# Performance work log

Measured on AMD Instinct MI355X. Metric: run time of the kernel, lower is better.

The kernel has to match this reference:

```python
import jax, jax.numpy as jnp
import numpy as np

T_STEPS = 40        # 30 gated steps + 10 extra steps (original while<30 then for min(10,..))
GATED_STEPS = 30
BATCH = 4096
X_DIM = 150
H_DIM = 150


def setup_inputs() -> dict:
    key = jax.random.key(0)
    ks = jax.random.split(key, 11)
    s = lambda k, shape: jax.random.normal(k, shape, jnp.float32) * 0.05
    return {
        "x": jax.random.normal(ks[0], (T_STEPS, BATCH, X_DIM), jnp.float32),
        "w_ih": s(ks[1], (4 * H_DIM, X_DIM)),
        "w_hh": s(ks[2], (4 * H_DIM, H_DIM)),
        "b_ih": s(ks[3], (4 * H_DIM,)),
        "b_hh": s(ks[4], (4 * H_DIM,)),
        "w1": s(ks[5], (50, X_DIM + H_DIM)),
        "b1": s(ks[6], (50,)),
        "w2": s(ks[7], (25, 50)),
        "b2": s(ks[8], (25,)),
        "w3": s(ks[9], (2, 25)),
        "b3": s(ks[10], (2,)),
    }


def reference(x, w_ih, w_hh, b_ih, b_hh, w1, b1, w2, b2, w3, b3):
    B = x.shape[1]
    H = w_hh.shape[1]

    def cell(h, c, xt):
        # PyTorch LSTMCell: gate order i, f, g, o
        g = xt @ w_ih.T + b_ih + h @ w_hh.T + b_hh  # [B, 4H]
        i, f, gg, o = jnp.split(g, 4, axis=-1)
        c = jax.nn.sigmoid(f) * c + jax.nn.sigmoid(i) * jnp.tanh(gg)
        h = jax.nn.sigmoid(o) * jnp.tanh(c)
        return h, c

    def stop_gate(h, xt):
        # original detaches the concat input (requires_grad=False on .data)
        t = jax.lax.stop_gradient(jnp.concatenate([h, xt], axis=-1))  # [B, 300]
        t = jax.nn.relu(t @ w1.T + b1)
        t = jax.nn.relu(t @ w2.T + b2)
        return jax.nn.softmax(jax.nn.relu(t @ w3.T + b3), axis=-1)  # [B, 2]

    def step_gated(carry, xt):
        h, c = carry
        h, c = cell(h, c, xt)
        y = stop_gate(h, xt)
        return (h, c), (h, y)

    def step_plain(carry, xt):
        h, c = carry
        h, c = cell(h, c, xt)
        return (h, c), h

    h0 = jnp.zeros((B, H), x.dtype)
    c0 = jnp.zeros((B, H), x.dtype)
    (h, c), (hs1, ys) = jax.lax.scan(step_gated, (h0, c0), x[:GATED_STEPS])
    outh = h  # h_t at the end of the gated phase (original `outh`)
    (h, c), hs2 = jax.lax.scan(step_plain, (h, c), x[GATED_STEPS:])
    outputs = jnp.concatenate([hs1, hs2], axis=0)  # [T, B, H]
    return outh, outputs, ys
```

## Files before the change

### kernel.cpp

```cpp
#include <hip/hip_runtime.h>
#include <math.h>

#define TSTEPS 40
#define GATED  30
#define BATCH  4096
#define XD     150
#define HD     150
#define HP     160
#define PITCHW 328
#define SXP    328
#define WROWS  704
#define ROWS   16
#define NT     512
#define NBLK   (BATCH / ROWS)

#define S1P    68
#define S2P    28
#define W2P    52

#define OFF_OUTPUTS 614400
#define OFF_YS      25190400

typedef float  floatx4 __attribute__((ext_vector_type(4)));
typedef short  shortx8 __attribute__((ext_vector_type(8)));

__device__ __forceinline__ unsigned short bf16_rne(float f) {
    union { float f; unsigned int u; } v; v.f = f;
    unsigned int u = v.u;
    return (unsigned short)((u + 0x7fffu + ((u >> 16) & 1u)) >> 16);
}
__device__ __forceinline__ unsigned int pk2bf(float a, float b) {
    return (unsigned int)bf16_rne(a) | ((unsigned int)bf16_rne(b) << 16);
}
__device__ __forceinline__ float rcp_f(float x) {
    return __builtin_amdgcn_rcpf(x);
}
__device__ __forceinline__ float sigf(float x) {
    return rcp_f(1.0f + __expf(-x));
}
__device__ __forceinline__ float tanh_fast(float x) {
    x = fminf(fmaxf(x, -15.0f), 15.0f);
    float t = __expf(2.0f * x);
    return (t - 1.0f) * rcp_f(t + 1.0f);
}
__device__ __forceinline__ void bar_lds() {
    asm volatile("s_waitcnt lgkmcnt(0)\n\ts_barrier" ::: "memory");
}

__global__ void pack_weights(const float* __restrict__ w_ih, const float* __restrict__ w_hh,
                             const float* __restrict__ b_ih, const float* __restrict__ b_hh,
                             const float* __restrict__ w1,
                             unsigned short* __restrict__ Wc, float* __restrict__ bcp) {
    int idx = blockIdx.x * blockDim.x + threadIdx.x;
    int stride = gridDim.x * blockDim.x;
    for (int i = idx; i < WROWS * PITCHW; i += stride) {
        int j = i / PITCHW, k = i - j * PITCHW;
        float v = 0.0f;
        if (j < 640) {
            int tp = j / HP, u = j - tp * HP;
            if (u < 150) {
                int src = tp * 150 + u;
                if (k < 150)                    v = w_ih[src * 150 + k];
                else if (k >= 160 && k < 310)   v = w_hh[src * 150 + (k - 160)];
            }
        } else {
            int j1 = j - 640;
            if (j1 < 50) {
                if (k < 150)                    v = w1[j1 * 300 + 150 + k];
                else if (k >= 160 && k < 310)   v = w1[j1 * 300 + (k - 160)];
            }
        }
        Wc[i] = bf16_rne(v);
    }
    for (int i = idx; i < 640; i += stride) {
        int tp = i / HP, u = i - tp * HP;
        bcp[i] = (u < 150) ? (b_ih[tp * 150 + u] + b_hh[tp * 150 + u]) : 0.0f;
    }
}

__global__ __launch_bounds__(NT, 2)
void lstm_main(const float* __restrict__ x,
               const unsigned short* __restrict__ Wc,
               const float* __restrict__ bcp,
               float* __restrict__ outh, float* __restrict__ outputs) {
    __shared__ unsigned short sxh[2][ROWS][SXP];
    __shared__ float sge[ROWS][4][33];
    __shared__ unsigned short wlds[8][16][SXP];
    __shared__ float bcs[640];

    const int tid  = threadIdx.x;
    const int lane = tid & 63;
    const int wv   = tid >> 6;
    const int lrow = lane & 15;
    const int lq   = lane >> 4;
    const int row0 = blockIdx.x * ROWS;
    const int ty   = wv >> 1;
    const int ch   = wv & 1;

    for (int i = tid; i < 2 * ROWS * SXP; i += NT) {
        int b = i / (ROWS * SXP);
        int rem = i - b * (ROWS * SXP);
        int r = rem / SXP, k = rem - r * SXP;
        if (k >= 150) sxh[b][r][k] = 0;
    }
    for (int i = tid; i < ROWS * 75; i += NT) {
        int rr = i / 75, kk = i - rr * 75;
        float2 v = *(const float2*)(x + ((size_t)row0 + rr) * XD + 2 * kk);
        *(unsigned int*)&sxh[0][rr][2 * kk] = pk2bf(v.x, v.y);
    }
    for (int i = tid; i < 8 * 16 * 160; i += NT) {
        int w = i / (16 * 160);
        int rem = i - w * (16 * 160);
        int r = rem / 160, k = rem - r * 160;
        int et = 10 * (w >> 1) + 8 + (w & 1);
        *(unsigned int*)&wlds[w][r][2 * k] =
            *(const unsigned int*)&Wc[(size_t)(et * 16 + r) * PITCHW + 2 * k];
    }
    for (int i = tid; i < 640; i += NT) bcs[i] = bcp[i];

    shortx8 bfr[40];
#pragma unroll
    for (int j = 0; j < 4; ++j) {
        const unsigned short* wp =
            Wc + (size_t)((10 * j + wv) * 16 + lrow) * PITCHW + lq * 8;
#pragma unroll
        for (int kb = 0; kb < 10; ++kb)
            bfr[j * 10 + kb] = *(const shortx8*)(wp + kb * 32);
    }

    __syncthreads();

    const int uq = wv * 16 + lrow;
    const float bcq0 = bcs[uq];
    const float bcq1 = bcs[160 + uq];
    const float bcq2 = bcs[320 + uq];
    const float bcq3 = bcs[480 + uq];
    const int ce_c = tid & 31;
    const int ue = 128 + ce_c;
    const int re = tid >> 5;
    const float bce0 = bcs[ue];
    const float bce1 = bcs[160 + ue];
    const float bce2 = bcs[320 + ue];
    const float bce3 = bcs[480 + ue];
    const int pr0 = tid / 75,          pk0 = tid % 75;
    const int pr1 = (tid + 512) / 75,  pk1 = (tid + 512) % 75;
    const int pr2 = (tid + 1024) / 75, pk2 = (tid + 1024) % 75;

    float* outc = outputs + (size_t)(row0 + lq * 4) * HD + uq;

    float cr[4] = {0.f, 0.f, 0.f, 0.f};
    float cex = 0.f;

    unsigned short (*sxc)[SXP] = sxh[0];
    unsigned short (*sxn)[SXP] = sxh[1];

    for (int t = 0; t < TSTEPS; ++t) {
        float2 px0, px1, px2;
        const bool pf = (t + 1 < TSTEPS);
        if (pf) {
            const float* xn = x + ((size_t)(t + 1) * BATCH + row0) * XD;
            px0 = *(const float2*)(xn + pr0 * XD + 2 * pk0);
            px1 = *(const float2*)(xn + pr1 * XD + 2 * pk1);
            if (tid < 176) px2 = *(const float2*)(xn + pr2 * XD + 2 * pk2);
        }

        float ge0, ge1, ge2, ge3;
        if (t > 0) {
            ge0 = sge[re][0][ce_c];
            ge1 = sge[re][1][ce_c];
            ge2 = sge[re][2][ce_c];
            ge3 = sge[re][3][ce_c];
        }

        floatx4 acc[5];
#pragma unroll
        for (int j = 0; j < 5; ++j) acc[j] = (floatx4){0.f, 0.f, 0.f, 0.f};
#pragma unroll
        for (int kb = 0; kb < 9; ++kb) {
            shortx8 a = *(const shortx8*)&sxc[lrow][kb * 32 + lq * 8];
#pragma unroll
            for (int j = 0; j < 4; ++j)
                acc[j] = __builtin_amdgcn_mfma_f32_16x16x32_bf16(
                    a, bfr[j * 10 + kb], acc[j], 0, 0, 0);
            shortx8 b4 = *(const shortx8*)&wlds[wv][lrow][kb * 32 + lq * 8];
            acc[4] = __builtin_amdgcn_mfma_f32_16x16x32_bf16(a, b4, acc[4], 0, 0, 0);
        }

        if (t > 0) {
            float gi = ge0 + bce0;
            float gf = ge1 + bce1;
            float gg = ge2 + bce2;
            float go = ge3 + bce3;
            float cn = sigf(gf) * cex + sigf(gi) * tanh_fast(gg);
            cex = cn;
            float h = sigf(go) * tanh_fast(cn);
            sxc[re][HP + ue] = bf16_rne(h);
            if (ue < 150) {
                outputs[((size_t)(t - 1) * BATCH + row0 + re) * HD + ue] = h;
                if (t == GATED)
                    outh[(size_t)(row0 + re) * HD + ue] = h;
            }
        }
        bar_lds();

        {
            shortx8 a = *(const shortx8*)&sxc[lrow][9 * 32 + lq * 8];
#pragma unroll
            for (int j = 0; j < 4; ++j)
                acc[j] = __builtin_amdgcn_mfma_f32_16x16x32_bf16(
                    a, bfr[j * 10 + 9], acc[j], 0, 0, 0);
            shortx8 b4 = *(const shortx8*)&wlds[wv][lrow][9 * 32 + lq * 8];
            acc[4] = __builtin_amdgcn_mfma_f32_16x16x32_bf16(a, b4, acc[4], 0, 0, 0);
        }

#pragma unroll
        for (int rg = 0; rg < 4; ++rg)
            sge[lq * 4 + rg][ty][ch * 16 + lrow] = acc[4][rg];

#pragma unroll
        for (int rg = 0; rg < 4; ++rg) {
            float gi = acc[0][rg] + bcq0;
            float gf = acc[1][rg] + bcq1;
            float gg = acc[2][rg] + bcq2;
            float go = acc[3][rg] + bcq3;
            float cn = sigf(gf) * cr[rg] + sigf(gi) * tanh_fast(gg);
            cr[rg] = cn;
            float h = sigf(go) * tanh_fast(cn);
            sxn[lq * 4 + rg][HP + uq] = bf16_rne(h);
            outc[rg * HD] = h;
            if (t == GATED - 1)
                outh[(size_t)(row0 + lq * 4 + rg) * HD + uq] = h;
        }
        if (pf) {
            *(unsigned int*)&sxn[pr0][2 * pk0] = pk2bf(px0.x, px0.y);
            *(unsigned int*)&sxn[pr1][2 * pk1] = pk2bf(px1.x, px1.y);
            if (tid < 176)
                *(unsigned int*)&sxn[pr2][2 * pk2] = pk2bf(px2.x, px2.y);
        }
        bar_lds();

        { unsigned short (*tmp)[SXP] = sxc; sxc = sxn; sxn = tmp; }
        outc += (size_t)BATCH * HD;
    }

    {
        float gi = sge[re][0][ce_c] + bce0;
        float gf = sge[re][1][ce_c] + bce1;
        float gg = sge[re][2][ce_c] + bce2;
        float go = sge[re][3][ce_c] + bce3;
        float cn = sigf(gf) * cex + sigf(gi) * tanh_fast(gg);
        float h = sigf(go) * tanh_fast(cn);
        if (ue < 150)
            outputs[((size_t)(TSTEPS - 1) * BATCH + row0 + re) * HD + ue] = h;
    }
}

#define SG_JOBS 4
__global__ __launch_bounds__(256, 2)
void stop_gate(const float* __restrict__ x,
               const unsigned short* __restrict__ Wc,
               const float* __restrict__ b1,
               const float* __restrict__ w2, const float* __restrict__ b2,
               const float* __restrict__ w3, const float* __restrict__ b3,
               const float* __restrict__ outputs, float* __restrict__ ys) {
    __shared__ unsigned short sA[64][SXP];
    __shared__ float st1[64][S1P];
    __shared__ float st2[64][S2P];
    __shared__ float sw2p[25][W2P];
    __shared__ float sw3p[2][S2P];
    __shared__ float b1s[64], sb2[25], sb3[2];

    const int tid  = threadIdx.x;
    const int lane = tid & 63;
    const int wv   = tid >> 6;
    const int lrow = lane & 15;
    const int lq   = lane >> 4;

    for (int i = tid; i < 64 * 10; i += 256) {
        int r = i / 10, c = i - r * 10;
        int col = (c < 5) ? (150 + 2 * c) : (310 + 2 * (c - 5));
        *(unsigned int*)&sA[r][col] = 0;
    }
    for (int i = tid; i < 64 * 3; i += 256)
        st2[i / 3][25 + i % 3] = 0.0f;
    for (int i = tid; i < 25 * W2P; i += 256) {
        int j = i / W2P, k = i - j * W2P;
        sw2p[j][k] = (k < 50) ? w2[j * 50 + k] : 0.0f;
    }
    if (tid < 2 * S2P) {
        int j = tid / S2P, k = tid - j * S2P;
        sw3p[j][k] = (k < 25) ? w3[j * 25 + k] : 0.0f;
    }
    if (tid < 64) b1s[tid] = (tid < 50) ? b1[tid] : 0.0f;
    if (tid < 25) sb2[tid] = b2[tid];
    if (tid < 2)  sb3[tid] = b3[tid];
    __syncthreads();

    for (int jb = 0; jb < SG_JOBS; ++jb) {
        const int job  = blockIdx.x * SG_JOBS + jb;
        const int t    = job >> 6;
        const int row0 = (job & 63) * 64;

        for (int i = tid; i < 64 * 75; i += 256) {
            int row = i / 75, kk = i - row * 75;
            size_t base = ((size_t)t * BATCH + row0 + row) * (size_t)XD;
            float2 xv = *(const float2*)(x + base + 2 * kk);
            float2 hv = *(const float2*)(outputs + base + 2 * kk);
            *(unsigned int*)&sA[row][2 * kk]      = pk2bf(xv.x, xv.y);
            *(unsigned int*)&sA[row][HP + 2 * kk] = pk2bf(hv.x, hv.y);
        }
        __syncthreads();

#pragma unroll
        for (int ct = 0; ct < 4; ++ct) {
            const unsigned short* wp1 =
                Wc + (size_t)(640 + ct * 16 + lrow) * PITCHW + lq * 8;
            floatx4 aw = {0.f, 0.f, 0.f, 0.f};
#pragma unroll
            for (int kb = 0; kb < 10; ++kb) {
                shortx8 a = *(const shortx8*)&sA[wv * 16 + lrow][kb * 32 + lq * 8];
                shortx8 b = *(const shortx8*)(wp1 + kb * 32);
                aw = __builtin_amdgcn_mfma_f32_16x16x32_bf16(a, b, aw, 0, 0, 0);
            }
#pragma unroll
            for (int rg = 0; rg < 4; ++rg)
                st1[wv * 16 + lq * 4 + rg][ct * 16 + lrow] = aw[rg];
        }
        __syncthreads();

        for (int e = tid; e < 64 * 64; e += 256) {
            int s = e >> 6, j = e & 63;
            float v = st1[s][j] + b1s[j];
            st1[s][j] = v > 0.0f ? v : 0.0f;
        }
        __syncthreads();

        for (int u = tid; u < 64 * 25; u += 256) {
            int s = u / 25, j = u - s * 25;
            float a = sb2[j];
#pragma unroll
            for (int m = 0; m < 13; ++m) {
                floatx4 a4 = *(const floatx4*)&st1[s][4 * m];
                floatx4 w4 = *(const floatx4*)&sw2p[j][4 * m];
                a = fmaf(w4[0], a4[0], a);
                a = fmaf(w4[1], a4[1], a);
                a = fmaf(w4[2], a4[2], a);
                a = fmaf(w4[3], a4[3], a);
            }
            st2[s][j] = a > 0.0f ? a : 0.0f;
        }
        __syncthreads();

        if (tid < 64) {
            float z0 = sb3[0], z1 = sb3[1];
#pragma unroll
            for (int m = 0; m < 7; ++m) {
                floatx4 a4 = *(const floatx4*)&st2[tid][4 * m];
                floatx4 w0 = *(const floatx4*)&sw3p[0][4 * m];
                floatx4 w1v = *(const floatx4*)&sw3p[1][4 * m];
                z0 = fmaf(w0[0], a4[0], z0);  z1 = fmaf(w1v[0], a4[0], z1);
                z0 = fmaf(w0[1], a4[1], z0);  z1 = fmaf(w1v[1], a4[1], z1);
                z0 = fmaf(w0[2], a4[2], z0);  z1 = fmaf(w1v[2], a4[2], z1);
                z0 = fmaf(w0[3], a4[3], z0);  z1 = fmaf(w1v[3], a4[3], z1);
            }
            z0 = z0 > 0.0f ? z0 : 0.0f;
            z1 = z1 > 0.0f ? z1 : 0.0f;
            float mx = fmaxf(z0, z1);
            float e0 = __expf(z0 - mx), e1 = __expf(z1 - mx);
            float inv = rcp_f(e0 + e1);
            float2 y = {e0 * inv, e1 * inv};
            *(float2*)&ys[((size_t)t * BATCH + row0 + tid) * 2] = y;
        }
        __syncthreads();
    }
}

extern "C" void kernel_launch(void* const* d_in, const int* in_sizes, int n_in,
                              void* d_out, int out_size, void* d_ws, size_t ws_size,
                              hipStream_t stream) {
    const float* x    = (const float*)d_in[0];
    const float* w_ih = (const float*)d_in[1];
    const float* w_hh = (const float*)d_in[2];
    const float* b_ih = (const float*)d_in[3];
    const float* b_hh = (const float*)d_in[4];
    const float* w1   = (const float*)d_in[5];
    const float* b1   = (const float*)d_in[6];
    const float* w2   = (const float*)d_in[7];
    const float* b2   = (const float*)d_in[8];
    const float* w3   = (const float*)d_in[9];
    const float* b3   = (const float*)d_in[10];

    float* out = (float*)d_out;
    unsigned short* Wc  = (unsigned short*)d_ws;
    float*          bcp = (float*)(Wc + WROWS * PITCHW);

    pack_weights<<<256, 256, 0, stream>>>(w_ih, w_hh, b_ih, b_hh, w1, Wc, bcp);

    lstm_main<<<NBLK, NT, 0, stream>>>(
        x, Wc, bcp, out, out + OFF_OUTPUTS);

    stop_gate<<<(GATED * 64) / SG_JOBS, 256, 0, stream>>>(
        x, Wc, b1, w2, b2, w3, b3, out + OFF_OUTPUTS, out + OFF_YS);
}
```

Before: 309.9 us.

## Split extra-tile weights between registers and LDS, fold bias into exp2, move outh write

Half of each wave's fifth-tile weights now live in registers, with only the recurrent half kept in a smaller LDS array. This cuts LDS footprint and load traffic in the recurrent loop. Gate activations use exp2 with the bias pre-scaled by log2e and fused into an FMA, and the output pointer for the extra columns is incremented instead of recomputed. The outh copy moves from the LSTM kernel into the stop-gate kernel. That kernel also fuses bias+ReLU into the MFMA epilogue and computes two layer-2 outputs per thread. These changes add register pressure under launch bounds of 2 and slightly change exp clamping.

```diff
diff --git a/kernel.cpp b/kernel.cpp
--- a/kernel.cpp
+++ b/kernel.cpp
@@ -9,6 +9,7 @@
 #define HP     160
 #define PITCHW 328
 #define SXP    328
+#define WLP    166
 #define WROWS  704
 #define ROWS   16
 #define NT     512
@@ -18,6 +19,8 @@
 #define S2P    28
 #define W2P    52
 
+#define LOG2E 1.44269504088896f
+
 #define OFF_OUTPUTS 614400
 #define OFF_YS      25190400
 
@@ -35,12 +38,18 @@
 __device__ __forceinline__ float rcp_f(float x) {
     return __builtin_amdgcn_rcpf(x);
 }
-__device__ __forceinline__ float sigf(float x) {
-    return rcp_f(1.0f + __expf(-x));
-}
-__device__ __forceinline__ float tanh_fast(float x) {
-    x = fminf(fmaxf(x, -15.0f), 15.0f);
-    float t = __expf(2.0f * x);
+__device__ __forceinline__ float sig2(float acc, float pb) {
+    return rcp_f(1.0f + exp2f(fmaf(acc, -LOG2E, pb)));
+}
+__device__ __forceinline__ float tanh2pre(float acc, float pb) {
+    float a = fmaf(acc, 2.0f * LOG2E, pb);
+    a = fminf(fmaxf(a, -44.0f), 44.0f);
+    float t = exp2f(a);
+    return (t - 1.0f) * rcp_f(t + 1.0f);
+}
+__device__ __forceinline__ float tanh2(float x) {
+    float a = fminf(fmaxf(2.0f * LOG2E * x, -44.0f), 44.0f);
+    float t = exp2f(a);
     return (t - 1.0f) * rcp_f(t + 1.0f);
 }
 __device__ __forceinline__ void bar_lds() {
@@ -82,10 +91,10 @@
 void lstm_main(const float* __restrict__ x,
                const unsigned short* __restrict__ Wc,
                const float* __restrict__ bcp,
-               float* __restrict__ outh, float* __restrict__ outputs) {
+               float* __restrict__ outputs) {
     __shared__ unsigned short sxh[2][ROWS][SXP];
     __shared__ float sge[ROWS][4][33];
-    __shared__ unsigned short wlds[8][16][SXP];
+    __shared__ unsigned short wldsh[8][16][WLP];
     __shared__ float bcs[640];
 
     const int tid  = threadIdx.x;
@@ -96,6 +105,7 @@
     const int row0 = blockIdx.x * ROWS;
     const int ty   = wv >> 1;
     const int ch   = wv & 1;
+    const int ET   = 10 * ty + 8 + ch;
 
     for (int i = tid; i < 2 * ROWS * SXP; i += NT) {
         int b = i / (ROWS * SXP);
@@ -108,13 +118,13 @@
         float2 v = *(const float2*)(x + ((size_t)row0 + rr) * XD + 2 * kk);
         *(unsigned int*)&sxh[0][rr][2 * kk] = pk2bf(v.x, v.y);
     }
-    for (int i = tid; i < 8 * 16 * 160; i += NT) {
-        int w = i / (16 * 160);
-        int rem = i - w * (16 * 160);
-        int r = rem / 160, k = rem - r * 160;
+    for (int i = tid; i < 8 * 16 * 80; i += NT) {
+        int w = i / (16 * 80);
+        int rem = i - w * (16 * 80);
+        int r = rem / 80, k = rem - r * 80;
         int et = 10 * (w >> 1) + 8 + (w & 1);
-        *(unsigned int*)&wlds[w][r][2 * k] =
-            *(const unsigned int*)&Wc[(size_t)(et * 16 + r) * PITCHW + 2 * k];
+        *(unsigned int*)&wldsh[w][r][2 * k] =
+            *(const unsigned int*)&Wc[(size_t)(et * 16 + r) * PITCHW + 160 + 2 * k];
     }
     for (int i = tid; i < 640; i += NT) bcs[i] = bcp[i];
 
@@ -127,26 +137,36 @@
         for (int kb = 0; kb < 10; ++kb)
             bfr[j * 10 + kb] = *(const shortx8*)(wp + kb * 32);
     }
+    shortx8 efx[5];
+    {
+        const unsigned short* wpe =
+            Wc + (size_t)(ET * 16 + lrow) * PITCHW + lq * 8;
+#pragma unroll
+        for (int kb = 0; kb < 5; ++kb)
+            efx[kb] = *(const shortx8*)(wpe + kb * 32);
+    }
 
     __syncthreads();
 
     const int uq = wv * 16 + lrow;
-    const float bcq0 = bcs[uq];
-    const float bcq1 = bcs[160 + uq];
-    const float bcq2 = bcs[320 + uq];
-    const float bcq3 = bcs[480 + uq];
+    const float bcq0s = -LOG2E * bcs[uq];
+    const float bcq1s = -LOG2E * bcs[160 + uq];
+    const float bcq2s = 2.0f * LOG2E * bcs[320 + uq];
+    const float bcq3s = -LOG2E * bcs[480 + uq];
     const int ce_c = tid & 31;
     const int ue = 128 + ce_c;
     const int re = tid >> 5;
-    const float bce0 = bcs[ue];
-    const float bce1 = bcs[160 + ue];
-    const float bce2 = bcs[320 + ue];
-    const float bce3 = bcs[480 + ue];
+    const float bce0s = -LOG2E * bcs[ue];
+    const float bce1s = -LOG2E * bcs[160 + ue];
+    const float bce2s = 2.0f * LOG2E * bcs[320 + ue];
+    const float bce3s = -LOG2E * bcs[480 + ue];
+    const bool  ewr   = (ue < 150);
     const int pr0 = tid / 75,          pk0 = tid % 75;
     const int pr1 = (tid + 512) / 75,  pk1 = (tid + 512) % 75;
     const int pr2 = (tid + 1024) / 75, pk2 = (tid + 1024) % 75;
 
     float* outc = outputs + (size_t)(row0 + lq * 4) * HD + uq;
+    float* oute = outputs + (size_t)(row0 + re) * HD + ue;
 
     float cr[4] = {0.f, 0.f, 0.f, 0.f};
     float cex = 0.f;
@@ -182,24 +202,21 @@
             for (int j = 0; j < 4; ++j)
                 acc[j] = __builtin_amdgcn_mfma_f32_16x16x32_bf16(
                     a, bfr[j * 10 + kb], acc[j], 0, 0, 0);
-            shortx8 b4 = *(const shortx8*)&wlds[wv][lrow][kb * 32 + lq * 8];
+            shortx8 b4 = (kb < 5) ? efx[kb]
+                : *(const shortx8*)&wldsh[wv][lrow][(kb - 5) * 32 + lq * 8];
             acc[4] = __builtin_amdgcn_mfma_f32_16x16x32_bf16(a, b4, acc[4], 0, 0, 0);
         }
 
         if (t > 0) {
-            float gi = ge0 + bce0;
-            float gf = ge1 + bce1;
-            float gg = ge2 + bce2;
-            float go = ge3 + bce3;
-            float cn = sigf(gf) * cex + sigf(gi) * tanh_fast(gg);
+            float si = sig2(ge0, bce0s);
+            float sf = sig2(ge1, bce1s);
+            float tg = tanh2pre(ge2, bce2s);
+            float so = sig2(ge3, bce3s);
+            float cn = sf * cex + si * tg;
             cex = cn;
-            float h = sigf(go) * tanh_fast(cn);
+            float h = so * tanh2(cn);
             sxc[re][HP + ue] = bf16_rne(h);
-            if (ue < 150) {
-                outputs[((size_t)(t - 1) * BATCH + row0 + re) * HD + ue] = h;
-                if (t == GATED)
-                    outh[(size_t)(row0 + re) * HD + ue] = h;
-            }
+            if (ewr) oute[0] = h;
         }
         bar_lds();
 
@@ -209,7 +226,7 @@
             for (int j = 0; j < 4; ++j)
                 acc[j] = __builtin_amdgcn_mfma_f32_16x16x32_bf16(
                     a, bfr[j * 10 + 9], acc[j], 0, 0, 0);
-            shortx8 b4 = *(const shortx8*)&wlds[wv][lrow][9 * 32 + lq * 8];
+            shortx8 b4 = *(const shortx8*)&wldsh[wv][lrow][4 * 32 + lq * 8];
             acc[4] = __builtin_amdgcn_mfma_f32_16x16x32_bf16(a, b4, acc[4], 0, 0, 0);
         }
 
@@ -219,17 +236,15 @@
 
 #pragma unroll
         for (int rg = 0; rg < 4; ++rg) {
-            float gi = acc[0][rg] + bcq0;
-            float gf = acc[1][rg] + bcq1;
-            float gg = acc[2][rg] + bcq2;
-            float go = acc[3][rg] + bcq3;
-            float cn = sigf(gf) * cr[rg] + sigf(gi) * tanh_fast(gg);
+            float si = sig2(acc[0][rg], bcq0s);
+            float sf = sig2(acc[1][rg], bcq1s);
+            float tg = tanh2pre(acc[2][rg], bcq2s);
+            float so = sig2(acc[3][rg], bcq3s);
+            float cn = sf * cr[rg] + si * tg;
             cr[rg] = cn;
-            float h = sigf(go) * tanh_fast(cn);
+            float h = so * tanh2(cn);
             sxn[lq * 4 + rg][HP + uq] = bf16_rne(h);
             outc[rg * HD] = h;
-            if (t == GATED - 1)
-                outh[(size_t)(row0 + lq * 4 + rg) * HD + uq] = h;
         }
         if (pf) {
             *(unsigned int*)&sxn[pr0][2 * pk0] = pk2bf(px0.x, px0.y);
@@ -241,17 +256,17 @@
 
         { unsigned short (*tmp)[SXP] = sxc; sxc = sxn; sxn = tmp; }
         outc += (size_t)BATCH * HD;
+        if (t > 0) oute += (size_t)BATCH * HD;
     }
 
     {
-        float gi = sge[re][0][ce_c] + bce0;
-        float gf = sge[re][1][ce_c] + bce1;
-        float gg = sge[re][2][ce_c] + bce2;
-        float go = sge[re][3][ce_c] + bce3;
-        float cn = sigf(gf) * cex + sigf(gi) * tanh_fast(gg);
-        float h = sigf(go) * tanh_fast(cn);
-        if (ue < 150)
-            outputs[((size_t)(TSTEPS - 1) * BATCH + row0 + re) * HD + ue] = h;
+        float si = sig2(sge[re][0][ce_c], bce0s);
+        float sf = sig2(sge[re][1][ce_c], bce1s);
+        float tg = tanh2pre(sge[re][2][ce_c], bce2s);
+        float so = sig2(sge[re][3][ce_c], bce3s);
+        float cn = sf * cex + si * tg;
+        float h = so * tanh2(cn);
+        if (ewr) oute[0] = h;
     }
 }
 
@@ -262,13 +277,14 @@
                const float* __restrict__ b1,
                const float* __restrict__ w2, const float* __restrict__ b2,
                const float* __restrict__ w3, const float* __restrict__ b3,
-               const float* __restrict__ outputs, float* __restrict__ ys) {
+               const float* __restrict__ outputs, float* __restrict__ outh,
+               float* __restrict__ ys) {
     __shared__ unsigned short sA[64][SXP];
     __shared__ float st1[64][S1P];
     __shared__ float st2[64][S2P];
-    __shared__ float sw2p[25][W2P];
+    __shared__ float sw2p[26][W2P];
     __shared__ float sw3p[2][S2P];
-    __shared__ float b1s[64], sb2[25], sb3[2];
+    __shared__ float b1s[64], sb2[26], sb3[2];
 
     const int tid  = threadIdx.x;
     const int lane = tid & 63;
@@ -283,16 +299,16 @@
     }
     for (int i = tid; i < 64 * 3; i += 256)
         st2[i / 3][25 + i % 3] = 0.0f;
-    for (int i = tid; i < 25 * W2P; i += 256) {
+    for (int i = tid; i < 26 * W2P; i += 256) {
         int j = i / W2P, k = i - j * W2P;
-        sw2p[j][k] = (k < 50) ? w2[j * 50 + k] : 0.0f;
+        sw2p[j][k] = (j < 25 && k < 50) ? w2[j * 50 + k] : 0.0f;
     }
     if (tid < 2 * S2P) {
         int j = tid / S2P, k = tid - j * S2P;
         sw3p[j][k] = (k < 25) ? w3[j * 25 + k] : 0.0f;
     }
     if (tid < 64) b1s[tid] = (tid < 50) ? b1[tid] : 0.0f;
-    if (tid < 25) sb2[tid] = b2[tid];
+    if (tid < 26) sb2[tid] = (tid < 25) ? b2[tid] : 0.0f;
     if (tid < 2)  sb3[tid] = b3[tid];
     __syncthreads();
 
@@ -308,6 +324,8 @@
             float2 hv = *(const float2*)(outputs + base + 2 * kk);
             *(unsigned int*)&sA[row][2 * kk]      = pk2bf(xv.x, xv.y);
             *(unsigned int*)&sA[row][HP + 2 * kk] = pk2bf(hv.x, hv.y);
+            if (t == GATED - 1)
+                *(float2*)&outh[(size_t)(row0 + row) * HD + 2 * kk] = hv;
         }
         __syncthreads();
 
@@ -322,32 +340,31 @@
                 shortx8 b = *(const shortx8*)(wp1 + kb * 32);
                 aw = __builtin_amdgcn_mfma_f32_16x16x32_bf16(a, b, aw, 0, 0, 0);
             }
-#pragma unroll
-            for (int rg = 0; rg < 4; ++rg)
-                st1[wv * 16 + lq * 4 + rg][ct * 16 + lrow] = aw[rg];
+            float bv = b1s[ct * 16 + lrow];
+#pragma unroll
+            for (int rg = 0; rg < 4; ++rg) {
+                float v = aw[rg] + bv;
+                st1[wv * 16 + lq * 4 + rg][ct * 16 + lrow] = v > 0.0f ? v : 0.0f;
+            }
         }
         __syncthreads();
 
-        for (int e = tid; e < 64 * 64; e += 256) {
-            int s = e >> 6, j = e & 63;
-            float v = st1[s][j] + b1s[j];
-            st1[s][j] = v > 0.0f ? v : 0.0f;
-        }
-        __syncthreads();
-
-        for (int u = tid; u < 64 * 25; u += 256) {
-            int s = u / 25, j = u - s * 25;
-            float a = sb2[j];
+        for (int u = tid; u < 64 * 13; u += 256) {
+            int s = u / 13, jp = u - s * 13;
+            int j0 = 2 * jp, j1 = j0 + 1;
+            float a0 = sb2[j0], a1 = sb2[j1];
 #pragma unroll
             for (int m = 0; m < 13; ++m) {
-                floatx4 a4 = *(const floatx4*)&st1[s][4 * m];
-                floatx4 w4 = *(const floatx4*)&sw2p[j][4 * m];
-                a = fmaf(w4[0], a4[0], a);
-                a = fmaf(w4[1], a4[1], a);
-                a = fmaf(w4[2], a4[2], a);
-                a = fmaf(w4[3], a4[3], a);
-            }
-            st2[s][j] = a > 0.0f ? a : 0.0f;
+                floatx4 a4  = *(const floatx4*)&st1[s][4 * m];
+                floatx4 w40 = *(const floatx4*)&sw2p[j0][4 * m];
+                floatx4 w41 = *(const floatx4*)&sw2p[j1][4 * m];
+                a0 = fmaf(w40[0], a4[0], a0);  a1 = fmaf(w41[0], a4[0], a1);
+                a0 = fmaf(w40[1], a4[1], a0);  a1 = fmaf(w41[1], a4[1], a1);
+                a0 = fmaf(w40[2], a4[2], a0);  a1 = fmaf(w41[2], a4[2], a1);
+                a0 = fmaf(w40[3], a4[3], a0);  a1 = fmaf(w41[3], a4[3], a1);
+            }
+            st2[s][j0] = a0 > 0.0f ? a0 : 0.0f;
+            st2[s][j1] = a1 > 0.0f ? a1 : 0.0f;
         }
         __syncthreads();
 
@@ -397,8 +414,8 @@
     pack_weights<<<256, 256, 0, stream>>>(w_ih, w_hh, b_ih, b_hh, w1, Wc, bcp);
 
     lstm_main<<<NBLK, NT, 0, stream>>>(
-        x, Wc, bcp, out, out + OFF_OUTPUTS);
+        x, Wc, bcp, out + OFF_OUTPUTS);
 
     stop_gate<<<(GATED * 64) / SG_JOBS, 256, 0, stream>>>(
-        x, Wc, b1, w2, b2, w3, b3, out + OFF_OUTPUTS, out + OFF_YS);
-}
+        x, Wc, b1, w2, b2, w3, b3, out + OFF_OUTPUTS, out, out + OFF_YS);
+}
```

After: 339.1 us. +9.4%, slower.
